# Kernel tuning notes

Hardware: AMD Instinct MI355X
Metric: run time of the kernel (lower is better)

## Reference

```python
import jax, jax.numpy as jnp
import numpy as np
import math

DIM = 1024
HEADS = 16
B, N = 2, 2048

POLY = jnp.array([-0.037, 0.481, -2.3, 4.917, -1.791], dtype=jnp.float32)


def adaptive_temperature_softmax(logits):
    # logits: [b, h, n, n]
    original_probs = jax.nn.softmax(logits, axis=-1)
    entropy = jnp.sum(-original_probs * jnp.log(original_probs + 1e-9), axis=-1, keepdims=True)
    e2 = entropy * entropy
    poly_result = POLY[0] * e2 * e2 + POLY[1] * e2 * entropy + POLY[2] * e2 + POLY[3] * entropy + POLY[4]
    beta = jnp.where(entropy > 0.5, jnp.maximum(poly_result, 1.0), 1.0)
    return jax.nn.softmax(logits * beta, axis=-1)


def setup_inputs() -> dict:
    key = jax.random.key(0)
    ks = jax.random.split(key, 5)
    s = 1.0 / math.sqrt(DIM)
    return {
        "x": jax.random.normal(ks[0], (B, N, DIM), dtype=jnp.float32),
        "Wq": jax.random.normal(ks[1], (DIM, DIM), dtype=jnp.float32) * s,
        "Wk": jax.random.normal(ks[2], (DIM, DIM), dtype=jnp.float32) * s,
        "Wv": jax.random.normal(ks[3], (DIM, DIM), dtype=jnp.float32) * s,
        "Wo": jax.random.normal(ks[4], (DIM, DIM), dtype=jnp.float32) * s,
        "bo": jnp.zeros((DIM,), dtype=jnp.float32),
    }


def reference(x, Wq, Wk, Wv, Wo, bo):
    b, n, d = x.shape
    h = HEADS
    hd = d // h
    # torch nn.Linear: y = x @ W.T (+ bias)
    def proj(W):
        t = x @ W.T  # [b, n, d]
        return t.reshape(b, n, h, hd).transpose(0, 2, 1, 3)  # [b, h, n, hd]
    q, k, v = proj(Wq), proj(Wk), proj(Wv)
    sim = jnp.einsum('bhid,bhjd->bhij', q, k) / math.sqrt(hd)
    neg = -jnp.finfo(sim.dtype).max
    causal = jnp.triu(jnp.ones((n, n), dtype=bool), k=1)  # True above diagonal
    sim = jnp.where(causal, neg, sim)
    attn = adaptive_temperature_softmax(sim)
    out = jnp.einsum('bhij,bhjd->bhid', attn, v)
    out = out.transpose(0, 2, 1, 3).reshape(b, n, d)
    return out @ Wo.T + bo
```

## Files before the change

kernel.cpp:

```cpp
#include <hip/hip_runtime.h>
#include <math.h>

#define B_   2
#define N_   2048
#define D_   1024
#define H_   16
#define HD_  64
#define BH_  32
#define M_   4096

typedef __bf16 bf16x8 __attribute__((ext_vector_type(8)));
typedef float  f32x4  __attribute__((ext_vector_type(4)));

__device__ inline unsigned short f2b(float f) {
    unsigned u = __float_as_uint(f);
    u += 0x7FFFu + ((u >> 16) & 1u);
    return (unsigned short)(u >> 16);
}
__device__ inline unsigned short f2b_fast(float f) {
    return (unsigned short)((__float_as_uint(f) + 0x8000u) >> 16);
}

__global__ __launch_bounds__(256)
void cvt_all(const float* __restrict__ x,  const float* __restrict__ wq,
             const float* __restrict__ wk, const float* __restrict__ wv,
             const float* __restrict__ wo, ushort* __restrict__ dst)
{
    int i = blockIdx.x * 256 + threadIdx.x;
    if (i >= 2097152) return;
    int fi = i * 4;
    const float* s; int off;
    if (fi < 4194304) { s = x; off = fi; }
    else {
        int r = fi - 4194304;
        int wsel = r >> 20;
        off = r & 1048575;
        s = (wsel == 0) ? wq : (wsel == 1) ? wk : (wsel == 2) ? wv : wo;
    }
    float4 f = *(const float4*)(s + off);
    ushort4 o;
    o.x = f2b(f.x); o.y = f2b(f.y); o.z = f2b(f.z); o.w = f2b(f.w);
    *(ushort4*)(dst + fi) = o;
}

__global__ __launch_bounds__(256)
void gemm_qkv(const ushort* __restrict__ A,
              const ushort* __restrict__ W0, const ushort* __restrict__ W1,
              const ushort* __restrict__ W2,
              ushort* __restrict__ O0, ushort* __restrict__ O1,
              ushort* __restrict__ O2)
{
    const int z = blockIdx.z;
    const ushort* W = (z == 0) ? W0 : (z == 1) ? W1 : W2;

    __shared__ alignas(16) ushort As[128][40];
    __shared__ alignas(16) ushort Bs[128][40];

    const int t = threadIdx.x;
    const int lane = t & 63, w = t >> 6;
    const int quad = lane >> 4, l15 = lane & 15;
    const int wm = (w >> 1) * 64, wn = (w & 1) * 64;
    const int tileM = blockIdx.x * 128, tileN = blockIdx.y * 128;

    const int r0 = t >> 2, r1 = 64 + (t >> 2);
    const int cg = (t & 3) * 8;
    const ushort* GA0 = A + (size_t)(tileM + r0) * D_ + cg;
    const ushort* GA1 = A + (size_t)(tileM + r1) * D_ + cg;
    const ushort* GB0 = W + (size_t)(tileN + r0) * D_ + cg;
    const ushort* GB1 = W + (size_t)(tileN + r1) * D_ + cg;

    f32x4 acc[4][4];
#pragma unroll
    for (int mt = 0; mt < 4; ++mt)
#pragma unroll
        for (int nt = 0; nt < 4; ++nt) acc[mt][nt] = (f32x4){0.f, 0.f, 0.f, 0.f};

    uint4 pa0 = *(const uint4*)GA0, pa1 = *(const uint4*)GA1;
    uint4 pb0 = *(const uint4*)GB0, pb1 = *(const uint4*)GB1;

    for (int k0 = 0; k0 < D_; k0 += 32) {
        __syncthreads();
        *(uint4*)&As[r0][cg] = pa0;
        *(uint4*)&As[r1][cg] = pa1;
        *(uint4*)&Bs[r0][cg] = pb0;
        *(uint4*)&Bs[r1][cg] = pb1;
        __syncthreads();
        if (k0 + 32 < D_) {
            pa0 = *(const uint4*)(GA0 + k0 + 32);
            pa1 = *(const uint4*)(GA1 + k0 + 32);
            pb0 = *(const uint4*)(GB0 + k0 + 32);
            pb1 = *(const uint4*)(GB1 + k0 + 32);
        }

        bf16x8 af[4], bf[4];
#pragma unroll
        for (int mt = 0; mt < 4; ++mt) af[mt] = *(const bf16x8*)&As[wm + mt * 16 + l15][quad * 8];
#pragma unroll
        for (int nt = 0; nt < 4; ++nt) bf[nt] = *(const bf16x8*)&Bs[wn + nt * 16 + l15][quad * 8];
#pragma unroll
        for (int mt = 0; mt < 4; ++mt)
#pragma unroll
            for (int nt = 0; nt < 4; ++nt)
                acc[mt][nt] = __builtin_amdgcn_mfma_f32_16x16x32_bf16(af[mt], bf[nt], acc[mt][nt], 0, 0, 0);
    }

    ushort* O = (z == 0) ? O0 : (z == 1) ? O1 : O2;
    const float scl = (z == 0) ? 0.18033688f : 1.0f;
#pragma unroll
    for (int mt = 0; mt < 4; ++mt)
#pragma unroll
        for (int nt = 0; nt < 4; ++nt) {
            if (z == 2) {
                int rg0 = tileM + wm + mt * 16 + quad * 4;
                int cgc = tileN + wn + nt * 16 + l15;
                int b = rg0 >> 11, n0 = rg0 & (N_ - 1);
                int h = cgc >> 6, dd = cgc & 63;
                ushort4 o4;
                o4.x = f2b(acc[mt][nt][0]); o4.y = f2b(acc[mt][nt][1]);
                o4.z = f2b(acc[mt][nt][2]); o4.w = f2b(acc[mt][nt][3]);
                *(ushort4*)&O[((size_t)((b * H_ + h) * HD_ + dd)) * N_ + n0] = o4;
            } else {
#pragma unroll
                for (int r = 0; r < 4; ++r) {
                    int rg = tileM + wm + mt * 16 + quad * 4 + r;
                    int cgc = tileN + wn + nt * 16 + l15;
                    int b = rg >> 11, n = rg & (N_ - 1);
                    int h = cgc >> 6, dd = cgc & 63;
                    O[(((size_t)(b * H_ + h)) * N_ + n) * HD_ + dd] = f2b(acc[mt][nt][r] * scl);
                }
            }
        }
}

__global__ __launch_bounds__(256)
void gemm_fin(const ushort* __restrict__ A, const ushort* __restrict__ W,
              const float* __restrict__ bias, float* __restrict__ Of)
{
    __shared__ alignas(16) ushort As[128][40];
    __shared__ alignas(16) ushort Bs[64][40];

    const int t = threadIdx.x;
    const int lane = t & 63, w = t >> 6;
    const int quad = lane >> 4, l15 = lane & 15;
    const int wm = (w >> 1) * 64, wn = (w & 1) * 32;
    const int tileM = blockIdx.x * 128, tileN = blockIdx.y * 64;

    const int r0 = t >> 2, r1 = 64 + (t >> 2);
    const int cg = (t & 3) * 8;
    const ushort* GA0 = A + (size_t)(tileM + r0) * D_ + cg;
    const ushort* GA1 = A + (size_t)(tileM + r1) * D_ + cg;
    const ushort* GB0 = W + (size_t)(tileN + r0) * D_ + cg;

    f32x4 acc[4][2];
#pragma unroll
    for (int mt = 0; mt < 4; ++mt)
#pragma unroll
        for (int nt = 0; nt < 2; ++nt) acc[mt][nt] = (f32x4){0.f, 0.f, 0.f, 0.f};

    uint4 pa0 = *(const uint4*)GA0, pa1 = *(const uint4*)GA1;
    uint4 pb0 = *(const uint4*)GB0;

    for (int k0 = 0; k0 < D_; k0 += 32) {
        __syncthreads();
        *(uint4*)&As[r0][cg] = pa0;
        *(uint4*)&As[r1][cg] = pa1;
        *(uint4*)&Bs[r0 & 63][cg] = pb0;
        __syncthreads();
        if (k0 + 32 < D_) {
            pa0 = *(const uint4*)(GA0 + k0 + 32);
            pa1 = *(const uint4*)(GA1 + k0 + 32);
            pb0 = *(const uint4*)(GB0 + k0 + 32);
        }

        bf16x8 af[4], bf[2];
#pragma unroll
        for (int mt = 0; mt < 4; ++mt) af[mt] = *(const bf16x8*)&As[wm + mt * 16 + l15][quad * 8];
#pragma unroll
        for (int nt = 0; nt < 2; ++nt) bf[nt] = *(const bf16x8*)&Bs[wn + nt * 16 + l15][quad * 8];
#pragma unroll
        for (int mt = 0; mt < 4; ++mt)
#pragma unroll
            for (int nt = 0; nt < 2; ++nt)
                acc[mt][nt] = __builtin_amdgcn_mfma_f32_16x16x32_bf16(af[mt], bf[nt], acc[mt][nt], 0, 0, 0);
    }

#pragma unroll
    for (int mt = 0; mt < 4; ++mt)
#pragma unroll
        for (int nt = 0; nt < 2; ++nt)
#pragma unroll
            for (int r = 0; r < 4; ++r) {
                int rg = tileM + wm + mt * 16 + quad * 4 + r;
                int cgc = tileN + wn + nt * 16 + l15;
                Of[(size_t)rg * D_ + cgc] = acc[mt][nt][r] + bias[cgc];
            }
}

__global__ __launch_bounds__(256)
void attn_mfma(const ushort* __restrict__ Q, const ushort* __restrict__ K,
               const ushort* __restrict__ VT, ushort* __restrict__ AO)
{
    const int bid = blockIdx.x;
    const int qt = 31 - (bid >> 5);
    const int bh = bid & 31;
    const size_t kvbase = (size_t)bh * N_ * HD_;

    __shared__ alignas(16) ushort Ks[128][72];
    __shared__ alignas(16) ushort Vs[64][136];
    __shared__ alignas(16) ushort Ps[4][4][296];

    const int t = threadIdx.x;
    const int lane = t & 63, w = t >> 6;
    const int quad = lane >> 4, l15 = lane & 15;
    const float SH2 = 11.5416913f;
    const float LN2 = 0.69314718f;

    const int skey = t >> 3;
    const int skc  = (t & 7) * 8;
    const ushort* KS = K + kvbase + (size_t)skey * HD_ + skc;
    const int vhd = t >> 4;
    const int vkc = (t & 15) * 8;
    const ushort* VS = VT + kvbase + (size_t)vhd * N_ + vkc;

    const int qrow = w * 16 + quad * 4;
    const int b = bh >> 4, h = bh & 15;
    const int nCh = (qt + 2) >> 1;

    bf16x8 aq0, aq1;
    {
        const size_t qr = kvbase + (size_t)(qt * 64 + w * 16 + l15) * HD_;
        aq0 = *(const bf16x8*)&Q[qr + quad * 8];
        aq1 = *(const bf16x8*)&Q[qr + 32 + quad * 8];
    }

    float ez[4] = {0.f, 0.f, 0.f, 0.f};
    float sz[4] = {0.f, 0.f, 0.f, 0.f};

    auto p1_tile = [&](const int nt) {
        f32x4 sv = (f32x4){-SH2, -SH2, -SH2, -SH2};
        __builtin_amdgcn_s_setprio(1);
        sv = __builtin_amdgcn_mfma_f32_16x16x32_bf16(aq0, *(const bf16x8*)&Ks[nt * 16 + l15][quad * 8], sv, 0, 0, 0);
        sv = __builtin_amdgcn_mfma_f32_16x16x32_bf16(aq1, *(const bf16x8*)&Ks[nt * 16 + l15][32 + quad * 8], sv, 0, 0, 0);
        __builtin_amdgcn_s_setprio(0);
#pragma unroll
        for (int r = 0; r < 4; ++r) {
            float sh = sv[r];
            float e = __builtin_amdgcn_exp2f(sh);
            ez[r] += e;
            sz[r] = fmaf(e, sh, sz[r]);
        }
    };
    auto p1_tile_mask = [&](const int nt, const int j) {
        f32x4 sv = (f32x4){-SH2, -SH2, -SH2, -SH2};
        __builtin_amdgcn_s_setprio(1);
        sv = __builtin_amdgcn_mfma_f32_16x16x32_bf16(aq0, *(const bf16x8*)&Ks[nt * 16 + l15][quad * 8], sv, 0, 0, 0);
        sv = __builtin_amdgcn_mfma_f32_16x16x32_bf16(aq1, *(const bf16x8*)&Ks[nt * 16 + l15][32 + quad * 8], sv, 0, 0, 0);
        __builtin_amdgcn_s_setprio(0);
        const int kc = j * 16 + l15;
#pragma unroll
        for (int r = 0; r < 4; ++r) {
            float sh = sv[r];
            float e = (kc <= qrow + r) ? __builtin_amdgcn_exp2f(sh) : 0.f;
            ez[r] += e;
            sz[r] = fmaf(e, sh, sz[r]);
        }
    };

    uint4 k0 = *(const uint4*)KS;
    uint4 k1 = *(const uint4*)(KS + 32 * HD_);
    uint4 k2 = *(const uint4*)(KS + 64 * HD_);
    uint4 k3 = *(const uint4*)(KS + 96 * HD_);
    const int nF1 = nCh - 1;
    for (int c = 0; c < nF1; ++c) {
        __syncthreads();
        *(uint4*)&Ks[skey][skc]      = k0;
        *(uint4*)&Ks[32 + skey][skc] = k1;
        *(uint4*)&Ks[64 + skey][skc] = k2;
        *(uint4*)&Ks[96 + skey][skc] = k3;
        __syncthreads();
        {
            const ushort* nb = KS + (size_t)(c + 1) * (128 * HD_);
            k0 = *(const uint4*)nb;
            k1 = *(const uint4*)(nb + 32 * HD_);
            k2 = *(const uint4*)(nb + 64 * HD_);
            k3 = *(const uint4*)(nb + 96 * HD_);
        }
#pragma unroll
        for (int nt = 0; nt < 8; ++nt) p1_tile(nt);
    }
    __syncthreads();
    *(uint4*)&Ks[skey][skc]      = k0;
    *(uint4*)&Ks[32 + skey][skc] = k1;
    *(uint4*)&Ks[64 + skey][skc] = k2;
    *(uint4*)&Ks[96 + skey][skc] = k3;
    __syncthreads();
    if (qt & 1) {
#pragma unroll
        for (int nt = 0; nt < 4; ++nt) p1_tile(nt);
#pragma unroll
        for (int j = 0; j < 4; ++j) p1_tile_mask(4 + j, j);
    } else {
#pragma unroll
        for (int j = 0; j < 4; ++j) p1_tile_mask(j, j);
    }

#pragma unroll
    for (int r = 0; r < 4; ++r) {
#pragma unroll
        for (int off = 1; off < 16; off <<= 1) {
            ez[r] += __shfl_xor(ez[r], off);
            sz[r] += __shfl_xor(sz[r], off);
        }
    }

    float bl[4];
#pragma unroll
    for (int r = 0; r < 4; ++r) {
        float Z = ez[r];
        float Hh = LN2 * (__builtin_amdgcn_logf(Z) - sz[r] / Z);
        float bb = 1.f;
        if (Hh > 0.5f) {
            float e2 = Hh * Hh;
            float pp = -0.037f * e2 * e2 + 0.481f * e2 * Hh - 2.3f * e2 + 4.917f * Hh - 1.791f;
            bb = fmaxf(pp, 1.f);
        }
        bl[r] = bb;
    }

    f32x4 ov[4];
#pragma unroll
    for (int nt = 0; nt < 4; ++nt) ov[nt] = (f32x4){0.f, 0.f, 0.f, 0.f};
    float zp[4] = {0.f, 0.f, 0.f, 0.f};

    auto do_half = [&](const int hh, const bool diag) {
        float wv[4][4];
#pragma unroll
        for (int nt = 0; nt < 4; ++nt) {
            f32x4 sv = (f32x4){-SH2, -SH2, -SH2, -SH2};
            __builtin_amdgcn_s_setprio(1);
            sv = __builtin_amdgcn_mfma_f32_16x16x32_bf16(aq0, *(const bf16x8*)&Ks[hh * 64 + nt * 16 + l15][quad * 8], sv, 0, 0, 0);
            sv = __builtin_amdgcn_mfma_f32_16x16x32_bf16(aq1, *(const bf16x8*)&Ks[hh * 64 + nt * 16 + l15][32 + quad * 8], sv, 0, 0, 0);
            __builtin_amdgcn_s_setprio(0);
#pragma unroll
            for (int r = 0; r < 4; ++r) {
                float e = __builtin_amdgcn_exp2f(bl[r] * sv[r]);
                wv[nt][r] = (!diag || (nt * 16 + l15 <= qrow + r)) ? e : 0.f;
            }
        }
#pragma unroll
        for (int nt = 0; nt < 4; ++nt)
#pragma unroll
            for (int r = 0; r < 4; ++r)
                Ps[w][quad][r * 72 + nt * 16 + l15] = f2b_fast(wv[nt][r]);
#pragma unroll
        for (int r = 0; r < 4; ++r)
            zp[r] += (wv[0][r] + wv[1][r]) + (wv[2][r] + wv[3][r]);

        bf16x8 pa0 = *(const bf16x8*)&Ps[w][l15 >> 2][(l15 & 3) * 72 + quad * 8];
        bf16x8 pa1 = *(const bf16x8*)&Ps[w][l15 >> 2][(l15 & 3) * 72 + 32 + quad * 8];
#pragma unroll
        for (int nt = 0; nt < 4; ++nt) {
            __builtin_amdgcn_s_setprio(1);
            ov[nt] = __builtin_amdgcn_mfma_f32_16x16x32_bf16(pa0, *(const bf16x8*)&Vs[nt * 16 + l15][hh * 64 + quad * 8], ov[nt], 0, 0, 0);
            ov[nt] = __builtin_amdgcn_mfma_f32_16x16x32_bf16(pa1, *(const bf16x8*)&Vs[nt * 16 + l15][hh * 64 + 32 + quad * 8], ov[nt], 0, 0, 0);
            __builtin_amdgcn_s_setprio(0);
        }
    };

    k0 = *(const uint4*)KS;
    k1 = *(const uint4*)(KS + 32 * HD_);
    k2 = *(const uint4*)(KS + 64 * HD_);
    k3 = *(const uint4*)(KS + 96 * HD_);
    uint4 v0 = *(const uint4*)VS;
    uint4 v1 = *(const uint4*)(VS + 16 * N_);
    uint4 v2 = *(const uint4*)(VS + 32 * N_);
    uint4 v3 = *(const uint4*)(VS + 48 * N_);

    const int nFull = qt >> 1;
    for (int c = 0; c < nFull; ++c) {
        __syncthreads();
        *(uint4*)&Ks[skey][skc]      = k0;
        *(uint4*)&Ks[32 + skey][skc] = k1;
        *(uint4*)&Ks[64 + skey][skc] = k2;
        *(uint4*)&Ks[96 + skey][skc] = k3;
        *(uint4*)&Vs[vhd][vkc]       = v0;
        *(uint4*)&Vs[16 + vhd][vkc]  = v1;
        *(uint4*)&Vs[32 + vhd][vkc]  = v2;
        *(uint4*)&Vs[48 + vhd][vkc]  = v3;
        __syncthreads();
        {
            const ushort* nk = KS + (size_t)(c + 1) * (128 * HD_);
            k0 = *(const uint4*)nk;
            k1 = *(const uint4*)(nk + 32 * HD_);
            k2 = *(const uint4*)(nk + 64 * HD_);
            k3 = *(const uint4*)(nk + 96 * HD_);
            const ushort* nv = VS + (c + 1) * 128;
            v0 = *(const uint4*)nv;
            v1 = *(const uint4*)(nv + 16 * N_);
            v2 = *(const uint4*)(nv + 32 * N_);
            v3 = *(const uint4*)(nv + 48 * N_);
        }
        do_half(0, false);
        do_half(1, false);
    }
    __syncthreads();
    *(uint4*)&Ks[skey][skc]      = k0;
    *(uint4*)&Ks[32 + skey][skc] = k1;
    *(uint4*)&Ks[64 + skey][skc] = k2;
    *(uint4*)&Ks[96 + skey][skc] = k3;
    *(uint4*)&Vs[vhd][vkc]       = v0;
    *(uint4*)&Vs[16 + vhd][vkc]  = v1;
    *(uint4*)&Vs[32 + vhd][vkc]  = v2;
    *(uint4*)&Vs[48 + vhd][vkc]  = v3;
    __syncthreads();
    if (qt & 1) {
        do_half(0, false);
        do_half(1, true);
    } else {
        do_half(0, true);
    }

#pragma unroll
    for (int r = 0; r < 4; ++r)
#pragma unroll
        for (int off = 1; off < 16; off <<= 1) zp[r] += __shfl_xor(zp[r], off);

#pragma unroll
    for (int r = 0; r < 4; ++r) {
        int qg = qt * 64 + w * 16 + quad * 4 + r;
        float inv = 1.f / zp[r];
        size_t rowoff = ((size_t)(b * N_ + qg)) * D_ + h * HD_;
#pragma unroll
        for (int nt = 0; nt < 4; ++nt)
            AO[rowoff + nt * 16 + l15] = f2b(ov[nt][r] * inv);
    }
}

extern "C" void kernel_launch(void* const* d_in, const int* in_sizes, int n_in,
                              void* d_out, int out_size, void* d_ws, size_t ws_size,
                              hipStream_t stream)
{
    const float* x  = (const float*)d_in[0];
    const float* Wq = (const float*)d_in[1];
    const float* Wk = (const float*)d_in[2];
    const float* Wv = (const float*)d_in[3];
    const float* Wo = (const float*)d_in[4];
    const float* bo = (const float*)d_in[5];
    float* out = (float*)d_out;

    ushort* ws  = (ushort*)d_ws;
    ushort* xb  = ws;
    ushort* wqb = ws + 4194304;
    ushort* wkb = ws + 5242880;
    ushort* wvb = ws + 6291456;
    ushort* wob = ws + 7340032;
    ushort* Qb  = ws + 8388608;
    ushort* Kb  = ws + 12582912;
    ushort* Vtb = ws + 16777216;
    ushort* aob = ws + 20971520;

    cvt_all<<<8192, 256, 0, stream>>>(x, Wq, Wk, Wv, Wo, xb);

    gemm_qkv<<<dim3(32, 8, 3), 256, 0, stream>>>(
        xb, wqb, wkb, wvb, Qb, Kb, Vtb);

    attn_mfma<<<dim3(1024), 256, 0, stream>>>(Qb, Kb, Vtb, aob);

    gemm_fin<<<dim3(32, 16), 256, 0, stream>>>(aob, wob, bo, out);
}
```

Before: 199.9 us.

## Read K and V fragments directly from global memory instead of LDS staging

Removes the shared-memory staging of K and V tiles, along with their register prefetch and the block-wide barriers, in both attention passes. Each wave now loads its MFMA operand fragments straight from global memory (relying on L1/L2 for reuse across the four waves), and the loops are restructured into per-64-key groups. This cuts LDS traffic and synchronisation, but every wave issues redundant global loads with no software prefetch, so latency may be exposed.

```diff
diff --git a/kernel.cpp b/kernel.cpp
--- a/kernel.cpp
+++ b/kernel.cpp
@@ -205,8 +205,6 @@
     const int bh = bid & 31;
     const size_t kvbase = (size_t)bh * N_ * HD_;
 
-    __shared__ alignas(16) ushort Ks[128][72];
-    __shared__ alignas(16) ushort Vs[64][136];
     __shared__ alignas(16) ushort Ps[4][4][296];
 
     const int t = threadIdx.x;
@@ -215,16 +213,11 @@
     const float SH2 = 11.5416913f;
     const float LN2 = 0.69314718f;
 
-    const int skey = t >> 3;
-    const int skc  = (t & 7) * 8;
-    const ushort* KS = K + kvbase + (size_t)skey * HD_ + skc;
-    const int vhd = t >> 4;
-    const int vkc = (t & 15) * 8;
-    const ushort* VS = VT + kvbase + (size_t)vhd * N_ + vkc;
-
     const int qrow = w * 16 + quad * 4;
     const int b = bh >> 4, h = bh & 15;
-    const int nCh = (qt + 2) >> 1;
+
+    const ushort* Kl = K + kvbase + (size_t)l15 * HD_ + quad * 8;
+    const ushort* Vl = VT + kvbase + (size_t)l15 * N_ + quad * 8;
 
     bf16x8 aq0, aq1;
     {
@@ -236,11 +229,11 @@
     float ez[4] = {0.f, 0.f, 0.f, 0.f};
     float sz[4] = {0.f, 0.f, 0.f, 0.f};
 
-    auto p1_tile = [&](const int nt) {
+    auto p1_tile = [&](const int kb) {
         f32x4 sv = (f32x4){-SH2, -SH2, -SH2, -SH2};
         __builtin_amdgcn_s_setprio(1);
-        sv = __builtin_amdgcn_mfma_f32_16x16x32_bf16(aq0, *(const bf16x8*)&Ks[nt * 16 + l15][quad * 8], sv, 0, 0, 0);
-        sv = __builtin_amdgcn_mfma_f32_16x16x32_bf16(aq1, *(const bf16x8*)&Ks[nt * 16 + l15][32 + quad * 8], sv, 0, 0, 0);
+        sv = __builtin_amdgcn_mfma_f32_16x16x32_bf16(aq0, *(const bf16x8*)(Kl + (size_t)kb * HD_), sv, 0, 0, 0);
+        sv = __builtin_amdgcn_mfma_f32_16x16x32_bf16(aq1, *(const bf16x8*)(Kl + (size_t)kb * HD_ + 32), sv, 0, 0, 0);
         __builtin_amdgcn_s_setprio(0);
 #pragma unroll
         for (int r = 0; r < 4; ++r) {
@@ -250,11 +243,11 @@
             sz[r] = fmaf(e, sh, sz[r]);
         }
     };
-    auto p1_tile_mask = [&](const int nt, const int j) {
+    auto p1_tile_mask = [&](const int kb, const int j) {
         f32x4 sv = (f32x4){-SH2, -SH2, -SH2, -SH2};
         __builtin_amdgcn_s_setprio(1);
-        sv = __builtin_amdgcn_mfma_f32_16x16x32_bf16(aq0, *(const bf16x8*)&Ks[nt * 16 + l15][quad * 8], sv, 0, 0, 0);
-        sv = __builtin_amdgcn_mfma_f32_16x16x32_bf16(aq1, *(const bf16x8*)&Ks[nt * 16 + l15][32 + quad * 8], sv, 0, 0, 0);
+        sv = __builtin_amdgcn_mfma_f32_16x16x32_bf16(aq0, *(const bf16x8*)(Kl + (size_t)kb * HD_), sv, 0, 0, 0);
+        sv = __builtin_amdgcn_mfma_f32_16x16x32_bf16(aq1, *(const bf16x8*)(Kl + (size_t)kb * HD_ + 32), sv, 0, 0, 0);
         __builtin_amdgcn_s_setprio(0);
         const int kc = j * 16 + l15;
 #pragma unroll
@@ -266,42 +259,17 @@
         }
     };
 
-    uint4 k0 = *(const uint4*)KS;
-    uint4 k1 = *(const uint4*)(KS + 32 * HD_);
-    uint4 k2 = *(const uint4*)(KS + 64 * HD_);
-    uint4 k3 = *(const uint4*)(KS + 96 * HD_);
-    const int nF1 = nCh - 1;
-    for (int c = 0; c < nF1; ++c) {
-        __syncthreads();
-        *(uint4*)&Ks[skey][skc]      = k0;
-        *(uint4*)&Ks[32 + skey][skc] = k1;
-        *(uint4*)&Ks[64 + skey][skc] = k2;
-        *(uint4*)&Ks[96 + skey][skc] = k3;
-        __syncthreads();
-        {
-            const ushort* nb = KS + (size_t)(c + 1) * (128 * HD_);
-            k0 = *(const uint4*)nb;
-            k1 = *(const uint4*)(nb + 32 * HD_);
-            k2 = *(const uint4*)(nb + 64 * HD_);
-            k3 = *(const uint4*)(nb + 96 * HD_);
-        }
-#pragma unroll
-        for (int nt = 0; nt < 8; ++nt) p1_tile(nt);
-    }
-    __syncthreads();
-    *(uint4*)&Ks[skey][skc]      = k0;
-    *(uint4*)&Ks[32 + skey][skc] = k1;
-    *(uint4*)&Ks[64 + skey][skc] = k2;
-    *(uint4*)&Ks[96 + skey][skc] = k3;
-    __syncthreads();
-    if (qt & 1) {
-#pragma unroll
-        for (int nt = 0; nt < 4; ++nt) p1_tile(nt);
-#pragma unroll
-        for (int j = 0; j < 4; ++j) p1_tile_mask(4 + j, j);
-    } else {
-#pragma unroll
-        for (int j = 0; j < 4; ++j) p1_tile_mask(j, j);
+    for (int g = 0; g < qt; ++g) {
+        const int kb = g * 64;
+        p1_tile(kb);
+        p1_tile(kb + 16);
+        p1_tile(kb + 32);
+        p1_tile(kb + 48);
+    }
+    {
+        const int kb = qt * 64;
+#pragma unroll
+        for (int j = 0; j < 4; ++j) p1_tile_mask(kb + j * 16, j);
     }
 
 #pragma unroll
@@ -332,14 +300,14 @@
     for (int nt = 0; nt < 4; ++nt) ov[nt] = (f32x4){0.f, 0.f, 0.f, 0.f};
     float zp[4] = {0.f, 0.f, 0.f, 0.f};
 
-    auto do_half = [&](const int hh, const bool diag) {
+    auto do_half = [&](const int kb, const bool diag) {
         float wv[4][4];
 #pragma unroll
         for (int nt = 0; nt < 4; ++nt) {
             f32x4 sv = (f32x4){-SH2, -SH2, -SH2, -SH2};
             __builtin_amdgcn_s_setprio(1);
-            sv = __builtin_amdgcn_mfma_f32_16x16x32_bf16(aq0, *(const bf16x8*)&Ks[hh * 64 + nt * 16 + l15][quad * 8], sv, 0, 0, 0);
-            sv = __builtin_amdgcn_mfma_f32_16x16x32_bf16(aq1, *(const bf16x8*)&Ks[hh * 64 + nt * 16 + l15][32 + quad * 8], sv, 0, 0, 0);
+            sv = __builtin_amdgcn_mfma_f32_16x16x32_bf16(aq0, *(const bf16x8*)(Kl + (size_t)(kb + nt * 16) * HD_), sv, 0, 0, 0);
+            sv = __builtin_amdgcn_mfma_f32_16x16x32_bf16(aq1, *(const bf16x8*)(Kl + (size_t)(kb + nt * 16) * HD_ + 32), sv, 0, 0, 0);
             __builtin_amdgcn_s_setprio(0);
 #pragma unroll
             for (int r = 0; r < 4; ++r) {
@@ -361,64 +329,14 @@
 #pragma unroll
         for (int nt = 0; nt < 4; ++nt) {
             __builtin_amdgcn_s_setprio(1);
-            ov[nt] = __builtin_amdgcn_mfma_f32_16x16x32_bf16(pa0, *(const bf16x8*)&Vs[nt * 16 + l15][hh * 64 + quad * 8], ov[nt], 0, 0, 0);
-            ov[nt] = __builtin_amdgcn_mfma_f32_16x16x32_bf16(pa1, *(const bf16x8*)&Vs[nt * 16 + l15][hh * 64 + 32 + quad * 8], ov[nt], 0, 0, 0);
+            ov[nt] = __builtin_amdgcn_mfma_f32_16x16x32_bf16(pa0, *(const bf16x8*)(Vl + (size_t)nt * 16 * N_ + kb), ov[nt], 0, 0, 0);
+            ov[nt] = __builtin_amdgcn_mfma_f32_16x16x32_bf16(pa1, *(const bf16x8*)(Vl + (size_t)nt * 16 * N_ + kb + 32), ov[nt], 0, 0, 0);
             __builtin_amdgcn_s_setprio(0);
         }
     };
 
-    k0 = *(const uint4*)KS;
-    k1 = *(const uint4*)(KS + 32 * HD_);
-    k2 = *(const uint4*)(KS + 64 * HD_);
-    k3 = *(const uint4*)(KS + 96 * HD_);
-    uint4 v0 = *(const uint4*)VS;
-    uint4 v1 = *(const uint4*)(VS + 16 * N_);
-    uint4 v2 = *(const uint4*)(VS + 32 * N_);
-    uint4 v3 = *(const uint4*)(VS + 48 * N_);
-
-    const int nFull = qt >> 1;
-    for (int c = 0; c < nFull; ++c) {
-        __syncthreads();
-        *(uint4*)&Ks[skey][skc]      = k0;
-        *(uint4*)&Ks[32 + skey][skc] = k1;
-        *(uint4*)&Ks[64 + skey][skc] = k2;
-        *(uint4*)&Ks[96 + skey][skc] = k3;
-        *(uint4*)&Vs[vhd][vkc]       = v0;
-        *(uint4*)&Vs[16 + vhd][vkc]  = v1;
-        *(uint4*)&Vs[32 + vhd][vkc]  = v2;
-        *(uint4*)&Vs[48 + vhd][vkc]  = v3;
-        __syncthreads();
-        {
-            const ushort* nk = KS + (size_t)(c + 1) * (128 * HD_);
-            k0 = *(const uint4*)nk;
-            k1 = *(const uint4*)(nk + 32 * HD_);
-            k2 = *(const uint4*)(nk + 64 * HD_);
-            k3 = *(const uint4*)(nk + 96 * HD_);
-            const ushort* nv = VS + (c + 1) * 128;
-            v0 = *(const uint4*)nv;
-            v1 = *(const uint4*)(nv + 16 * N_);
-            v2 = *(const uint4*)(nv + 32 * N_);
-            v3 = *(const uint4*)(nv + 48 * N_);
-        }
-        do_half(0, false);
-        do_half(1, false);
-    }
-    __syncthreads();
-    *(uint4*)&Ks[skey][skc]      = k0;
-    *(uint4*)&Ks[32 + skey][skc] = k1;
-    *(uint4*)&Ks[64 + skey][skc] = k2;
-    *(uint4*)&Ks[96 + skey][skc] = k3;
-    *(uint4*)&Vs[vhd][vkc]       = v0;
-    *(uint4*)&Vs[16 + vhd][vkc]  = v1;
-    *(uint4*)&Vs[32 + vhd][vkc]  = v2;
-    *(uint4*)&Vs[48 + vhd][vkc]  = v3;
-    __syncthreads();
-    if (qt & 1) {
-        do_half(0, false);
-        do_half(1, true);
-    } else {
-        do_half(0, true);
-    }
+    for (int g = 0; g < qt; ++g) do_half(g * 64, false);
+    do_half(qt * 64, true);
 
 #pragma unroll
     for (int r = 0; r < 4; ++r)
```

New measurement: 355.9 us. 1.78x slower.

## Load V operands directly from global into registers, dropping V shared-memory staging

Applied to the files above, without the earlier changes.

The V tile is no longer staged through LDS. Each lane now loads its MFMA B-operand fragments for V straight from global memory into registers and double-buffers them (va/vb), prefetching the next 64-key block while the current one is used. This removes the LDS writes and reads for V and shrinks shared memory per block, which may raise occupancy. In exchange each of the four waves loads the full V block separately, so global/L2 traffic for V rises about 4x, and register pressure grows from 16 extra bf16x8 registers.

```diff
diff --git a/kernel.cpp b/kernel.cpp
--- a/kernel.cpp
+++ b/kernel.cpp
@@ -206,7 +206,6 @@
     const size_t kvbase = (size_t)bh * N_ * HD_;
 
     __shared__ alignas(16) ushort Ks[128][72];
-    __shared__ alignas(16) ushort Vs[64][136];
     __shared__ alignas(16) ushort Ps[4][4][296];
 
     const int t = threadIdx.x;
@@ -218,9 +217,7 @@
     const int skey = t >> 3;
     const int skc  = (t & 7) * 8;
     const ushort* KS = K + kvbase + (size_t)skey * HD_ + skc;
-    const int vhd = t >> 4;
-    const int vkc = (t & 15) * 8;
-    const ushort* VS = VT + kvbase + (size_t)vhd * N_ + vkc;
+    const ushort* Vl = VT + kvbase + (size_t)l15 * N_ + quad * 8;
 
     const int qrow = w * 16 + quad * 4;
     const int b = bh >> 4, h = bh & 15;
@@ -332,7 +329,20 @@
     for (int nt = 0; nt < 4; ++nt) ov[nt] = (f32x4){0.f, 0.f, 0.f, 0.f};
     float zp[4] = {0.f, 0.f, 0.f, 0.f};
 
-    auto do_half = [&](const int hh, const bool diag) {
+    bf16x8 va[8], vb[8];
+#pragma unroll
+    for (int f = 0; f < 8; ++f)
+        va[f] = *(const bf16x8*)(Vl + (size_t)(f >> 1) * 16 * N_ + (f & 1) * 32);
+
+    auto do_half = [&](const int kb, const int hh, const bool diag,
+                       const bf16x8 (&vcur)[8], bf16x8 (&vnxt)[8]) {
+        if (!diag) {
+            const int kbn = kb + 64;
+#pragma unroll
+            for (int f = 0; f < 8; ++f)
+                vnxt[f] = *(const bf16x8*)(Vl + (size_t)(f >> 1) * 16 * N_ + kbn + (f & 1) * 32);
+        }
+
         float wv[4][4];
 #pragma unroll
         for (int nt = 0; nt < 4; ++nt) {
@@ -361,8 +371,8 @@
 #pragma unroll
         for (int nt = 0; nt < 4; ++nt) {
             __builtin_amdgcn_s_setprio(1);
-            ov[nt] = __builtin_amdgcn_mfma_f32_16x16x32_bf16(pa0, *(const bf16x8*)&Vs[nt * 16 + l15][hh * 64 + quad * 8], ov[nt], 0, 0, 0);
-            ov[nt] = __builtin_amdgcn_mfma_f32_16x16x32_bf16(pa1, *(const bf16x8*)&Vs[nt * 16 + l15][hh * 64 + 32 + quad * 8], ov[nt], 0, 0, 0);
+            ov[nt] = __builtin_amdgcn_mfma_f32_16x16x32_bf16(pa0, vcur[nt * 2],     ov[nt], 0, 0, 0);
+            ov[nt] = __builtin_amdgcn_mfma_f32_16x16x32_bf16(pa1, vcur[nt * 2 + 1], ov[nt], 0, 0, 0);
             __builtin_amdgcn_s_setprio(0);
         }
     };
@@ -371,10 +381,6 @@
     k1 = *(const uint4*)(KS + 32 * HD_);
     k2 = *(const uint4*)(KS + 64 * HD_);
     k3 = *(const uint4*)(KS + 96 * HD_);
-    uint4 v0 = *(const uint4*)VS;
-    uint4 v1 = *(const uint4*)(VS + 16 * N_);
-    uint4 v2 = *(const uint4*)(VS + 32 * N_);
-    uint4 v3 = *(const uint4*)(VS + 48 * N_);
 
     const int nFull = qt >> 1;
     for (int c = 0; c < nFull; ++c) {
@@ -383,10 +389,6 @@
         *(uint4*)&Ks[32 + skey][skc] = k1;
         *(uint4*)&Ks[64 + skey][skc] = k2;
         *(uint4*)&Ks[96 + skey][skc] = k3;
-        *(uint4*)&Vs[vhd][vkc]       = v0;
-        *(uint4*)&Vs[16 + vhd][vkc]  = v1;
-        *(uint4*)&Vs[32 + vhd][vkc]  = v2;
-        *(uint4*)&Vs[48 + vhd][vkc]  = v3;
         __syncthreads();
         {
             const ushort* nk = KS + (size_t)(c + 1) * (128 * HD_);
@@ -394,30 +396,21 @@
             k1 = *(const uint4*)(nk + 32 * HD_);
             k2 = *(const uint4*)(nk + 64 * HD_);
             k3 = *(const uint4*)(nk + 96 * HD_);
-            const ushort* nv = VS + (c + 1) * 128;
-            v0 = *(const uint4*)nv;
-            v1 = *(const uint4*)(nv + 16 * N_);
-            v2 = *(const uint4*)(nv + 32 * N_);
-            v3 = *(const uint4*)(nv + 48 * N_);
-        }
-        do_half(0, false);
-        do_half(1, false);
+        }
+        do_half(c * 128,      0, false, va, vb);
+        do_half(c * 128 + 64, 1, false, vb, va);
     }
     __syncthreads();
     *(uint4*)&Ks[skey][skc]      = k0;
     *(uint4*)&Ks[32 + skey][skc] = k1;
     *(uint4*)&Ks[64 + skey][skc] = k2;
     *(uint4*)&Ks[96 + skey][skc] = k3;
-    *(uint4*)&Vs[vhd][vkc]       = v0;
-    *(uint4*)&Vs[16 + vhd][vkc]  = v1;
-    *(uint4*)&Vs[32 + vhd][vkc]  = v2;
-    *(uint4*)&Vs[48 + vhd][vkc]  = v3;
     __syncthreads();
     if (qt & 1) {
-        do_half(0, false);
-        do_half(1, true);
+        do_half((qt - 1) * 64, 0, false, va, vb);
+        do_half(qt * 64,       1, true,  vb, va);
     } else {
-        do_half(0, true);
+        do_half(qt * 64,       0, true,  va, vb);
     }
 
 #pragma unroll
```

New measurement: 237.5 us. 1.19x slower.

## Use 128-row query tiles with 8 waves per attention block

Applied to the files above, without the earlier changes.

The attention kernel now uses 512-thread blocks, each covering 128 query rows with 8 waves, so every K/V chunk loaded into shared memory is reused by twice as many queries and the grid shrinks to 512 blocks. The causal diagonal chunk is handled per wave: fully unmasked tiles skip the mask, the single diagonal tile is masked, and tiles above the diagonal are skipped entirely. Block order is reshuffled to interleave heavy and light query tiles, and the shared-memory row padding is reduced. The narrower padding makes LDS row strides no longer 16-byte multiples, so vector LDS reads may become misaligned, and larger blocks may reduce occupancy.

```diff
diff --git a/kernel.cpp b/kernel.cpp
--- a/kernel.cpp
+++ b/kernel.cpp
@@ -196,18 +196,19 @@
             }
 }
 
-__global__ __launch_bounds__(256)
+__global__ __launch_bounds__(512)
 void attn_mfma(const ushort* __restrict__ Q, const ushort* __restrict__ K,
                const ushort* __restrict__ VT, ushort* __restrict__ AO)
 {
     const int bid = blockIdx.x;
-    const int qt = 31 - (bid >> 5);
+    const int i16 = bid >> 5;
+    const int qt = (i16 < 8) ? (15 - i16) : (i16 - 8);
     const int bh = bid & 31;
     const size_t kvbase = (size_t)bh * N_ * HD_;
 
-    __shared__ alignas(16) ushort Ks[128][72];
-    __shared__ alignas(16) ushort Vs[64][136];
-    __shared__ alignas(16) ushort Ps[4][4][296];
+    __shared__ alignas(16) ushort Ks[128][68];
+    __shared__ alignas(16) ushort Vs[64][132];
+    __shared__ alignas(16) ushort Ps[8][4][288];
 
     const int t = threadIdx.x;
     const int lane = t & 63, w = t >> 6;
@@ -222,13 +223,13 @@
     const int vkc = (t & 15) * 8;
     const ushort* VS = VT + kvbase + (size_t)vhd * N_ + vkc;
 
-    const int qrow = w * 16 + quad * 4;
+    const int qr4 = quad * 4;
     const int b = bh >> 4, h = bh & 15;
-    const int nCh = (qt + 2) >> 1;
+    const int qbase = qt * 128;
 
     bf16x8 aq0, aq1;
     {
-        const size_t qr = kvbase + (size_t)(qt * 64 + w * 16 + l15) * HD_;
+        const size_t qr = kvbase + (size_t)(qbase + w * 16 + l15) * HD_;
         aq0 = *(const bf16x8*)&Q[qr + quad * 8];
         aq1 = *(const bf16x8*)&Q[qr + 32 + quad * 8];
     }
@@ -250,58 +251,44 @@
             sz[r] = fmaf(e, sh, sz[r]);
         }
     };
-    auto p1_tile_mask = [&](const int nt, const int j) {
+    auto p1_tile_mask = [&](const int nt) {
         f32x4 sv = (f32x4){-SH2, -SH2, -SH2, -SH2};
         __builtin_amdgcn_s_setprio(1);
         sv = __builtin_amdgcn_mfma_f32_16x16x32_bf16(aq0, *(const bf16x8*)&Ks[nt * 16 + l15][quad * 8], sv, 0, 0, 0);
         sv = __builtin_amdgcn_mfma_f32_16x16x32_bf16(aq1, *(const bf16x8*)&Ks[nt * 16 + l15][32 + quad * 8], sv, 0, 0, 0);
         __builtin_amdgcn_s_setprio(0);
-        const int kc = j * 16 + l15;
 #pragma unroll
         for (int r = 0; r < 4; ++r) {
             float sh = sv[r];
-            float e = (kc <= qrow + r) ? __builtin_amdgcn_exp2f(sh) : 0.f;
+            float e = (l15 <= qr4 + r) ? __builtin_amdgcn_exp2f(sh) : 0.f;
             ez[r] += e;
             sz[r] = fmaf(e, sh, sz[r]);
         }
     };
 
     uint4 k0 = *(const uint4*)KS;
-    uint4 k1 = *(const uint4*)(KS + 32 * HD_);
-    uint4 k2 = *(const uint4*)(KS + 64 * HD_);
-    uint4 k3 = *(const uint4*)(KS + 96 * HD_);
-    const int nF1 = nCh - 1;
-    for (int c = 0; c < nF1; ++c) {
+    uint4 k1 = *(const uint4*)(KS + 64 * HD_);
+    for (int c = 0; c < qt; ++c) {
         __syncthreads();
         *(uint4*)&Ks[skey][skc]      = k0;
-        *(uint4*)&Ks[32 + skey][skc] = k1;
-        *(uint4*)&Ks[64 + skey][skc] = k2;
-        *(uint4*)&Ks[96 + skey][skc] = k3;
+        *(uint4*)&Ks[64 + skey][skc] = k1;
         __syncthreads();
         {
             const ushort* nb = KS + (size_t)(c + 1) * (128 * HD_);
             k0 = *(const uint4*)nb;
-            k1 = *(const uint4*)(nb + 32 * HD_);
-            k2 = *(const uint4*)(nb + 64 * HD_);
-            k3 = *(const uint4*)(nb + 96 * HD_);
+            k1 = *(const uint4*)(nb + 64 * HD_);
         }
 #pragma unroll
         for (int nt = 0; nt < 8; ++nt) p1_tile(nt);
     }
     __syncthreads();
     *(uint4*)&Ks[skey][skc]      = k0;
-    *(uint4*)&Ks[32 + skey][skc] = k1;
-    *(uint4*)&Ks[64 + skey][skc] = k2;
-    *(uint4*)&Ks[96 + skey][skc] = k3;
+    *(uint4*)&Ks[64 + skey][skc] = k1;
     __syncthreads();
-    if (qt & 1) {
-#pragma unroll
-        for (int nt = 0; nt < 4; ++nt) p1_tile(nt);
-#pragma unroll
-        for (int j = 0; j < 4; ++j) p1_tile_mask(4 + j, j);
-    } else {
-#pragma unroll
-        for (int j = 0; j < 4; ++j) p1_tile_mask(j, j);
+#pragma unroll
+    for (int j = 0; j < 8; ++j) {
+        if (j < w)       p1_tile(j);
+        else if (j == w) p1_tile_mask(j);
     }
 
 #pragma unroll
@@ -332,7 +319,7 @@
     for (int nt = 0; nt < 4; ++nt) ov[nt] = (f32x4){0.f, 0.f, 0.f, 0.f};
     float zp[4] = {0.f, 0.f, 0.f, 0.f};
 
-    auto do_half = [&](const int hh, const bool diag) {
+    auto do_half = [&](const int hh) {
         float wv[4][4];
 #pragma unroll
         for (int nt = 0; nt < 4; ++nt) {
@@ -342,10 +329,8 @@
             sv = __builtin_amdgcn_mfma_f32_16x16x32_bf16(aq1, *(const bf16x8*)&Ks[hh * 64 + nt * 16 + l15][32 + quad * 8], sv, 0, 0, 0);
             __builtin_amdgcn_s_setprio(0);
 #pragma unroll
-            for (int r = 0; r < 4; ++r) {
-                float e = __builtin_amdgcn_exp2f(bl[r] * sv[r]);
-                wv[nt][r] = (!diag || (nt * 16 + l15 <= qrow + r)) ? e : 0.f;
-            }
+            for (int r = 0; r < 4; ++r)
+                wv[nt][r] = __builtin_amdgcn_exp2f(bl[r] * sv[r]);
         }
 #pragma unroll
         for (int nt = 0; nt < 4; ++nt)
@@ -366,59 +351,88 @@
             __builtin_amdgcn_s_setprio(0);
         }
     };
+    auto do_half_diag = [&](const int hh) {
+        const int tbase = hh * 4;
+        if (w < tbase) return;
+        float wv[4][4];
+#pragma unroll
+        for (int nt = 0; nt < 4; ++nt) {
+            const int tc = tbase + nt;
+            if (tc < w) {
+                f32x4 sv = (f32x4){-SH2, -SH2, -SH2, -SH2};
+                __builtin_amdgcn_s_setprio(1);
+                sv = __builtin_amdgcn_mfma_f32_16x16x32_bf16(aq0, *(const bf16x8*)&Ks[hh * 64 + nt * 16 + l15][quad * 8], sv, 0, 0, 0);
+                sv = __builtin_amdgcn_mfma_f32_16x16x32_bf16(aq1, *(const bf16x8*)&Ks[hh * 64 + nt * 16 + l15][32 + quad * 8], sv, 0, 0, 0);
+                __builtin_amdgcn_s_setprio(0);
+#pragma unroll
+                for (int r = 0; r < 4; ++r)
+                    wv[nt][r] = __builtin_amdgcn_exp2f(bl[r] * sv[r]);
+            } else if (tc == w) {
+                f32x4 sv = (f32x4){-SH2, -SH2, -SH2, -SH2};
+                __builtin_amdgcn_s_setprio(1);
+                sv = __builtin_amdgcn_mfma_f32_16x16x32_bf16(aq0, *(const bf16x8*)&Ks[hh * 64 + nt * 16 + l15][quad * 8], sv, 0, 0, 0);
+                sv = __builtin_amdgcn_mfma_f32_16x16x32_bf16(aq1, *(const bf16x8*)&Ks[hh * 64 + nt * 16 + l15][32 + quad * 8], sv, 0, 0, 0);
+                __builtin_amdgcn_s_setprio(0);
+#pragma unroll
+                for (int r = 0; r < 4; ++r) {
+                    float e = __builtin_amdgcn_exp2f(bl[r] * sv[r]);
+                    wv[nt][r] = (l15 <= qr4 + r) ? e : 0.f;
+                }
+            } else {
+#pragma unroll
+                for (int r = 0; r < 4; ++r) wv[nt][r] = 0.f;
+            }
+        }
+#pragma unroll
+        for (int nt = 0; nt < 4; ++nt)
+#pragma unroll
+            for (int r = 0; r < 4; ++r)
+                Ps[w][quad][r * 72 + nt * 16 + l15] = f2b_fast(wv[nt][r]);
+#pragma unroll
+        for (int r = 0; r < 4; ++r)
+            zp[r] += (wv[0][r] + wv[1][r]) + (wv[2][r] + wv[3][r]);
+
+        bf16x8 pa0 = *(const bf16x8*)&Ps[w][l15 >> 2][(l15 & 3) * 72 + quad * 8];
+        bf16x8 pa1 = *(const bf16x8*)&Ps[w][l15 >> 2][(l15 & 3) * 72 + 32 + quad * 8];
+#pragma unroll
+        for (int nt = 0; nt < 4; ++nt) {
+            __builtin_amdgcn_s_setprio(1);
+            ov[nt] = __builtin_amdgcn_mfma_f32_16x16x32_bf16(pa0, *(const bf16x8*)&Vs[nt * 16 + l15][hh * 64 + quad * 8], ov[nt], 0, 0, 0);
+            ov[nt] = __builtin_amdgcn_mfma_f32_16x16x32_bf16(pa1, *(const bf16x8*)&Vs[nt * 16 + l15][hh * 64 + 32 + quad * 8], ov[nt], 0, 0, 0);
+            __builtin_amdgcn_s_setprio(0);
+        }
+    };
 
     k0 = *(const uint4*)KS;
-    k1 = *(const uint4*)(KS + 32 * HD_);
-    k2 = *(const uint4*)(KS + 64 * HD_);
-    k3 = *(const uint4*)(KS + 96 * HD_);
+    k1 = *(const uint4*)(KS + 64 * HD_);
     uint4 v0 = *(const uint4*)VS;
-    uint4 v1 = *(const uint4*)(VS + 16 * N_);
-    uint4 v2 = *(const uint4*)(VS + 32 * N_);
-    uint4 v3 = *(const uint4*)(VS + 48 * N_);
-
-    const int nFull = qt >> 1;
-    for (int c = 0; c < nFull; ++c) {
+    uint4 v1 = *(const uint4*)(VS + 32 * N_);
+    for (int c = 0; c < qt; ++c) {
         __syncthreads();
         *(uint4*)&Ks[skey][skc]      = k0;
-        *(uint4*)&Ks[32 + skey][skc] = k1;
-        *(uint4*)&Ks[64 + skey][skc] = k2;
-        *(uint4*)&Ks[96 + skey][skc] = k3;
+        *(uint4*)&Ks[64 + skey][skc] = k1;
         *(uint4*)&Vs[vhd][vkc]       = v0;
-        *(uint4*)&Vs[16 + vhd][vkc]  = v1;
-        *(uint4*)&Vs[32 + vhd][vkc]  = v2;
-        *(uint4*)&Vs[48 + vhd][vkc]  = v3;
+        *(uint4*)&Vs[32 + vhd][vkc]  = v1;
         __syncthreads();
         {
             const ushort* nk = KS + (size_t)(c + 1) * (128 * HD_);
             k0 = *(const uint4*)nk;
-            k1 = *(const uint4*)(nk + 32 * HD_);
-            k2 = *(const uint4*)(nk + 64 * HD_);
-            k3 = *(const uint4*)(nk + 96 * HD_);
+            k1 = *(const uint4*)(nk + 64 * HD_);
             const ushort* nv = VS + (c + 1) * 128;
             v0 = *(const uint4*)nv;
-            v1 = *(const uint4*)(nv + 16 * N_);
-            v2 = *(const uint4*)(nv + 32 * N_);
-            v3 = *(const uint4*)(nv + 48 * N_);
-        }
-        do_half(0, false);
-        do_half(1, false);
+            v1 = *(const uint4*)(nv + 32 * N_);
+        }
+        do_half(0);
+        do_half(1);
     }
     __syncthreads();
     *(uint4*)&Ks[skey][skc]      = k0;
-    *(uint4*)&Ks[32 + skey][skc] = k1;
-    *(uint4*)&Ks[64 + skey][skc] = k2;
-    *(uint4*)&Ks[96 + skey][skc] = k3;
+    *(uint4*)&Ks[64 + skey][skc] = k1;
     *(uint4*)&Vs[vhd][vkc]       = v0;
-    *(uint4*)&Vs[16 + vhd][vkc]  = v1;
-    *(uint4*)&Vs[32 + vhd][vkc]  = v2;
-    *(uint4*)&Vs[48 + vhd][vkc]  = v3;
+    *(uint4*)&Vs[32 + vhd][vkc]  = v1;
     __syncthreads();
-    if (qt & 1) {
-        do_half(0, false);
-        do_half(1, true);
-    } else {
-        do_half(0, true);
-    }
+    do_half_diag(0);
+    do_half_diag(1);
 
 #pragma unroll
     for (int r = 0; r < 4; ++r)
@@ -427,7 +441,7 @@
 
 #pragma unroll
     for (int r = 0; r < 4; ++r) {
-        int qg = qt * 64 + w * 16 + quad * 4 + r;
+        int qg = qbase + w * 16 + qr4 + r;
         float inv = 1.f / zp[r];
         size_t rowoff = ((size_t)(b * N_ + qg)) * D_ + h * HD_;
 #pragma unroll
@@ -464,7 +478,7 @@
     gemm_qkv<<<dim3(32, 8, 3), 256, 0, stream>>>(
         xb, wqb, wkb, wvb, Qb, Kb, Vtb);
 
-    attn_mfma<<<dim3(1024), 256, 0, stream>>>(Qb, Kb, Vtb, aob);
+    attn_mfma<<<dim3(512), 512, 0, stream>>>(Qb, Kb, Vtb, aob);
 
     gemm_fin<<<dim3(32, 16), 256, 0, stream>>>(aob, wob, bo, out);
 }
```

New measurement: 219.0 us. 9.6% more time.
